# Optimization experiments

Measured on AMD Instinct MI355X. Metric: run time of the kernel, lower is better.

## Reference

```python
import jax, jax.numpy as jnp
import numpy as np

NUM_BLOCKS = 8
HIDDEN_FACTOR = 1
LAMBD = 0.01
HARD_FRACTION = 1.0
SCALE = 0.02


def softshrink(v, lambd):
    return jnp.sign(v) * jnp.maximum(jnp.abs(v) - lambd, 0.0)


def setup_inputs() -> dict:
    key = jax.random.key(0)
    ks = jax.random.split(key, 5)
    B, H, W, C = 4, 128, 128, 768
    bs = C // NUM_BLOCKS
    x = jax.random.normal(ks[0], (B, H * W, C), dtype=jnp.float32)
    w1 = SCALE * jax.random.normal(ks[1], (2, NUM_BLOCKS, bs, bs * HIDDEN_FACTOR), dtype=jnp.float32)
    b1 = SCALE * jax.random.normal(ks[2], (2, NUM_BLOCKS, bs * HIDDEN_FACTOR), dtype=jnp.float32)
    w2 = SCALE * jax.random.normal(ks[3], (2, NUM_BLOCKS, bs * HIDDEN_FACTOR, bs), dtype=jnp.float32)
    b2 = SCALE * jax.random.normal(ks[4], (2, NUM_BLOCKS, bs), dtype=jnp.float32)
    return {"x": x, "w1": w1, "b1": b1, "w2": w2, "b2": b2, "H": H, "W": W}


def reference(x, w1, b1, w2, b2, H, W):
    B, N, C = x.shape
    bs = C // NUM_BLOCKS
    bias = x
    xf = x.astype(jnp.float32).reshape(B, H, W, C)
    x_fft = jnp.fft.rfft2(xf, axes=(1, 2), norm='ortho')  # [B,H,W//2+1,C]
    Wm = W // 2 + 1
    kept = max(1, int(Wm * HARD_FRACTION))
    xr = x_fft.real.reshape(B, H, Wm, NUM_BLOCKS, bs)
    xi = x_fft.imag.reshape(B, H, Wm, NUM_BLOCKS, bs)
    xr_k = xr[:, :, :kept]
    xi_k = xi[:, :, :kept]
    # block-diagonal complex layer 1 + relu
    o1r = jax.nn.relu(jnp.einsum('bhwni,nio->bhwno', xr_k, w1[0])
                      - jnp.einsum('bhwni,nio->bhwno', xi_k, w1[1]) + b1[0])
    o1i = jax.nn.relu(jnp.einsum('bhwni,nio->bhwno', xi_k, w1[0])
                      + jnp.einsum('bhwni,nio->bhwno', xr_k, w1[1]) + b1[1])
    # layer 2
    o2r = (jnp.einsum('bhwno,noi->bhwni', o1r, w2[0])
           - jnp.einsum('bhwno,noi->bhwni', o1i, w2[1]) + b2[0])
    o2i = (jnp.einsum('bhwno,noi->bhwni', o1i, w2[0])
           + jnp.einsum('bhwno,noi->bhwni', o1r, w2[1]) + b2[1])
    o2r = softshrink(o2r, LAMBD)
    o2i = softshrink(o2i, LAMBD)
    # zero-pad unkept modes (kept == Wm when HARD_FRACTION == 1.0)
    if kept < Wm:
        pad = [(0, 0), (0, 0), (0, Wm - kept), (0, 0), (0, 0)]
        o2r = jnp.pad(o2r, pad)
        o2i = jnp.pad(o2i, pad)
    x_c = (o2r + 1j * o2i).reshape(B, H, Wm, C)
    x_out = jnp.fft.irfft2(x_c, s=(H, W), axes=(1, 2), norm='ortho')
    return x_out.reshape(B, N, C).astype(bias.dtype) + bias
```

## Files before the change

kernel.cpp:

```cpp
#include <hip/hip_runtime.h>
#include <hip/hip_bf16.h>

#define BDIM 256
constexpr int Bc = 4, Hc = 128, Wcn = 128, Cc = 768, WM = 65, NB = 8, BS = 96;
constexpr int NROWS = Bc * WM * Hc;
constexpr size_t NSPEC = (size_t)NROWS * Cc;

typedef __attribute__((ext_vector_type(8))) _Float16 f16x8;
typedef __attribute__((ext_vector_type(4))) float f32x4;
typedef __attribute__((ext_vector_type(4))) unsigned int u32x4;

__device__ __forceinline__ unsigned short f2h(float f) {
    return __builtin_bit_cast(unsigned short, (_Float16)f);
}
__device__ __forceinline__ float h2f(unsigned short s) {
    return (float)__builtin_bit_cast(_Float16, s);
}
__device__ __forceinline__ void barx() {
    __builtin_amdgcn_sched_barrier(0);
    asm volatile("s_waitcnt lgkmcnt(0)" ::: "memory");
    __builtin_amdgcn_s_barrier();
    __builtin_amdgcn_sched_barrier(0);
    asm volatile("" ::: "memory");
}

__global__ __launch_bounds__(BDIM) void kprep(const float* __restrict__ w1,
                                              const float* __restrict__ w2,
                                              unsigned short* __restrict__ WTg) {
    int idx = blockIdx.x * BDIM + threadIdx.x;
    if (idx >= 294912) return;
    int k = idx % 96, n = (idx / 96) % 96, blk = (idx / 9216) % 8, mat = idx / 73728;
    const float* src = (mat < 2) ? w1 : w2;
    int q = mat & 1;
    WTg[idx] = f2h(src[(((size_t)q * 8 + blk) * 96 + k) * 96 + n]);
}

constexpr int K1PAD = 136;
__global__ __launch_bounds__(BDIM, 1) void k1m(const float* __restrict__ x,
                                               unsigned short* __restrict__ Rr,
                                               unsigned short* __restrict__ Ri) {
    __shared__ unsigned short Xt[64][K1PAD];
    const int tid = threadIdx.x;
    const int lane = tid & 63;
    const int wv = tid >> 6;
    const int b = blockIdx.x >> 7, h = blockIdx.x & 127;
    const float* xp = x + ((size_t)(b * 16384 + h * 128)) * 768;
    const size_t sbase = ((size_t)(b * WM) * 128 + h) * 768;

    f16x8 Af[2][4];
    {
        const int rlo = wv * 32 + (lane & 15);
        #pragma unroll
        for (int rf = 0; rf < 2; ++rf) {
            const int r = rlo + rf * 16;
            const int m = (r < 65) ? r : (r - 64);
            #pragma unroll
            for (int ks = 0; ks < 4; ++ks) {
                f16x8 v;
                #pragma unroll
                for (int j = 0; j < 8; ++j) {
                    int k = ks * 32 + ((lane >> 4) << 3) + j;
                    float th = (float)((m * k) & 127) * 0.04908738521234052f;
                    float s, c; __sincosf(th, &s, &c);
                    v[j] = (_Float16)(((r < 65) ? c : -s) * 0.0078125f);
                }
                Af[rf][ks] = v;
            }
        }
    }

    const int w = tid & 127, cg = tid >> 7;
    float4 pfv[8];
    #pragma unroll
    for (int q = 0; q < 8; ++q)
        pfv[q] = *(const float4*)(xp + (size_t)w * 768 + cg * 32 + q * 4);

    const int koff = (lane >> 4) << 3;

    for (int t = 0; t < 12; ++t) {
        #pragma unroll
        for (int q = 0; q < 8; ++q) {
            float4 v = pfv[q];
            int cb = cg * 32 + q * 4;
            Xt[cb + 0][w] = f2h(v.x);
            Xt[cb + 1][w] = f2h(v.y);
            Xt[cb + 2][w] = f2h(v.z);
            Xt[cb + 3][w] = f2h(v.w);
        }
        if (t < 11) {
            #pragma unroll
            for (int q = 0; q < 8; ++q)
                pfv[q] = *(const float4*)(xp + (size_t)w * 768 + (t + 1) * 64 + cg * 32 + q * 4);
        }
        barx();

        f32x4 acc[2][4];
        #pragma unroll
        for (int rf = 0; rf < 2; ++rf)
            #pragma unroll
            for (int cf = 0; cf < 4; ++cf)
                acc[rf][cf] = (f32x4){0, 0, 0, 0};
        #pragma unroll
        for (int ks = 0; ks < 4; ++ks) {
            #pragma unroll
            for (int cf = 0; cf < 4; ++cf) {
                const int cl = cf * 16 + (lane & 15);
                f16x8 Bf = *(const f16x8*)(&Xt[cl][ks * 32 + koff]);
                #pragma unroll
                for (int rf = 0; rf < 2; ++rf)
                    acc[rf][cf] = __builtin_amdgcn_mfma_f32_16x16x32_f16(Af[rf][ks], Bf, acc[rf][cf], 0, 0, 0);
            }
        }
        #pragma unroll
        for (int rf = 0; rf < 2; ++rf)
            #pragma unroll
            for (int cf = 0; cf < 4; ++cf) {
                int col = t * 64 + cf * 16 + (lane & 15);
                int r0 = wv * 32 + rf * 16 + ((lane >> 4) << 2);
                #pragma unroll
                for (int reg = 0; reg < 4; ++reg) {
                    int r = r0 + reg;
                    if (r < 65) {
                        Rr[sbase + (size_t)r * 98304 + col] = f2h(acc[rf][cf][reg]);
                        if (r == 0)  Ri[sbase + col] = 0;
                        if (r == 64) Ri[sbase + (size_t)64 * 98304 + col] = 0;
                    } else {
                        Ri[sbase + (size_t)(r - 64) * 98304 + col] = f2h(acc[rf][cf][reg]);
                    }
                }
            }
        barx();
    }
}

constexpr int KMT = 136;
__global__ __launch_bounds__(BDIM) void kmid(unsigned short* __restrict__ Rr,
                                             unsigned short* __restrict__ Ri,
                                             const unsigned short* __restrict__ WTg,
                                             const float* __restrict__ b1,
                                             const float* __restrict__ b2) {
    extern __shared__ unsigned short lds[];
    unsigned short* Xtr = lds;
    unsigned short* Xti = Xtr + 96 * KMT;
    unsigned short* Y   = lds;

    const int tid = threadIdx.x;
    const int lane = tid & 63;
    const int wv = tid >> 6;
    const int blk = blockIdx.y;
    const size_t sbase = (size_t)blockIdx.x * 98304;

    const int hme = tid & 127, cgme = tid >> 7;
    u32x4 pfs[12];
    #pragma unroll
    for (int p = 0; p < 12; ++p) {
        const unsigned short* src = (p >= 6) ? Ri : Rr;
        int cg = (p % 6) * 2 + cgme;
        pfs[p] = *(const u32x4*)(src + sbase + (size_t)hme * 768 + blk * 96 + cg * 8);
    }

    const int n0 = wv * 48;
    float bias1[3], bias2[3];
    #pragma unroll
    for (int c = 0; c < 3; ++c) {
        int n = n0 + c * 16 + (lane & 15);
        bias1[c] = (n < 96) ? b1[blk * 96 + n] : b1[768 + blk * 96 + (n - 96)];
        bias2[c] = (n < 96) ? b2[blk * 96 + n] : b2[768 + blk * 96 + (n - 96)];
    }

    const int arow0 = wv * 32 + (lane & 15);
    const int koff = (lane >> 4) << 3;
    const int rowoff = (lane >> 4) << 2;

    int nq_c[3], nl_c[3];
    #pragma unroll
    for (int c = 0; c < 3; ++c) {
        nq_c[c] = (n0 + c * 16) < 96;
        nl_c[c] = n0 + c * 16 + (lane & 15) - (nq_c[c] ? 0 : 96);
    }

    #pragma unroll
    for (int p = 0; p < 12; ++p) {
        unsigned short* dst = (p >= 6) ? Xti : Xtr;
        int cl = ((p % 6) * 2 + cgme) * 8;
        unsigned short tmp[8];
        *(u32x4*)&tmp[0] = pfs[p];
        #pragma unroll
        for (int j = 0; j < 8; ++j)
            dst[(cl + j) * KMT + hme] = tmp[j];
    }
    __syncthreads();

    f32x4 accr[2][6], acci[2][6];
    #pragma unroll
    for (int rf = 0; rf < 2; ++rf)
        #pragma unroll
        for (int cf = 0; cf < 6; ++cf) {
            accr[rf][cf] = (f32x4){0, 0, 0, 0};
            acci[rf][cf] = (f32x4){0, 0, 0, 0};
        }
    {
        f16x8 Ca[2][4], Sa[2][4];
        #pragma unroll
        for (int rf = 0; rf < 2; ++rf) {
            const int r = arow0 + rf * 16;
            #pragma unroll
            for (int ks = 0; ks < 4; ++ks) {
                f16x8 cv, sv;
                #pragma unroll
                for (int j = 0; j < 8; ++j) {
                    int k = ks * 32 + koff + j;
                    float th = (float)((r * k) & 127) * 0.04908738521234052f;
                    float s, c; __sincosf(th, &s, &c);
                    cv[j] = (_Float16)c;
                    sv[j] = (_Float16)s;
                }
                Ca[rf][ks] = cv;
                Sa[rf][ks] = sv;
            }
        }
        #pragma unroll
        for (int ks = 0; ks < 4; ++ks) {
            f16x8 Sn[2];
            #pragma unroll
            for (int rf = 0; rf < 2; ++rf) {
                u32x4 u = __builtin_bit_cast(u32x4, Sa[rf][ks]);
                u ^= 0x80008000u;
                Sn[rf] = __builtin_bit_cast(f16x8, u);
            }
            #pragma unroll
            for (int cf = 0; cf < 6; ++cf) {
                int boff = (cf * 16 + (lane & 15)) * KMT + ks * 32 + koff;
                f16x8 Br = *(const f16x8*)(Xtr + boff);
                f16x8 Bi = *(const f16x8*)(Xti + boff);
                #pragma unroll
                for (int rf = 0; rf < 2; ++rf) {
                    accr[rf][cf] = __builtin_amdgcn_mfma_f32_16x16x32_f16(Ca[rf][ks], Br, accr[rf][cf], 0, 0, 0);
                    accr[rf][cf] = __builtin_amdgcn_mfma_f32_16x16x32_f16(Sa[rf][ks], Bi, accr[rf][cf], 0, 0, 0);
                    acci[rf][cf] = __builtin_amdgcn_mfma_f32_16x16x32_f16(Ca[rf][ks], Bi, acci[rf][cf], 0, 0, 0);
                    acci[rf][cf] = __builtin_amdgcn_mfma_f32_16x16x32_f16(Sn[rf], Br, acci[rf][cf], 0, 0, 0);
                }
            }
        }
    }
    __syncthreads();

    #pragma unroll
    for (int rf = 0; rf < 2; ++rf)
        #pragma unroll
        for (int cf = 0; cf < 6; ++cf) {
            int c = cf * 16 + (lane & 15);
            #pragma unroll
            for (int reg = 0; reg < 4; ++reg) {
                int row = wv * 32 + rf * 16 + rowoff + reg;
                Y[row * 200 + c]      = f2h(accr[rf][cf][reg]);
                Y[row * 200 + 96 + c] = f2h(acci[rf][cf][reg]);
            }
        }
    __syncthreads();

    const unsigned short* Xl = Y + (lane & 15) * 200 + koff;
    f32x4 acc[8][3];
    #pragma unroll
    for (int r = 0; r < 8; ++r)
        #pragma unroll
        for (int c = 0; c < 3; ++c)
            acc[r][c] = (f32x4){bias1[c], bias1[c], bias1[c], bias1[c]};
    #pragma unroll
    for (int kit = 0; kit < 6; ++kit) {
        const int kq = kit < 3;
        const int kl = kit * 32 + koff - (kq ? 0 : 96);
        f16x8 Bf[3];
        #pragma unroll
        for (int c = 0; c < 3; ++c) {
            const int quad = kq ? (nq_c[c] ? 0 : 1) : (nq_c[c] ? 1 : 0);
            f16x8 v = *(const f16x8*)(WTg + ((size_t)(quad * 8 + blk) * 96 + nl_c[c]) * 96 + kl);
            if ((!kq) && nq_c[c]) { u32x4 u = __builtin_bit_cast(u32x4, v); u ^= 0x80008000u; v = __builtin_bit_cast(f16x8, u); }
            Bf[c] = v;
        }
        f16x8 A[8];
        #pragma unroll
        for (int r = 0; r < 8; ++r)
            A[r] = *(const f16x8*)(Xl + r * 3200 + kit * 32);
        #pragma unroll
        for (int r = 0; r < 8; ++r)
            #pragma unroll
            for (int c = 0; c < 3; ++c)
                acc[r][c] = __builtin_amdgcn_mfma_f32_16x16x32_f16(A[r], Bf[c], acc[r][c], 0, 0, 0);
    }
    __syncthreads();
    #pragma unroll
    for (int r = 0; r < 8; ++r)
        #pragma unroll
        for (int c = 0; c < 3; ++c) {
            int ncol = n0 + c * 16 + (lane & 15);
            #pragma unroll
            for (int reg = 0; reg < 4; ++reg) {
                int row = r * 16 + rowoff + reg;
                Y[row * 200 + ncol] = f2h(fmaxf(acc[r][c][reg], 0.f));
            }
        }
    __syncthreads();

    #pragma unroll
    for (int r = 0; r < 8; ++r)
        #pragma unroll
        for (int c = 0; c < 3; ++c)
            acc[r][c] = (f32x4){bias2[c], bias2[c], bias2[c], bias2[c]};
    #pragma unroll
    for (int kit = 0; kit < 6; ++kit) {
        const int kq = kit < 3;
        const int kl = kit * 32 + koff - (kq ? 0 : 96);
        f16x8 Bf[3];
        #pragma unroll
        for (int c = 0; c < 3; ++c) {
            const int quad = kq ? (nq_c[c] ? 0 : 1) : (nq_c[c] ? 1 : 0);
            f16x8 v = *(const f16x8*)(WTg + ((size_t)((2 + quad) * 8 + blk) * 96 + nl_c[c]) * 96 + kl);
            if ((!kq) && nq_c[c]) { u32x4 u = __builtin_bit_cast(u32x4, v); u ^= 0x80008000u; v = __builtin_bit_cast(f16x8, u); }
            Bf[c] = v;
        }
        f16x8 A[8];
        #pragma unroll
        for (int r = 0; r < 8; ++r)
            A[r] = *(const f16x8*)(Xl + r * 3200 + kit * 32);
        #pragma unroll
        for (int r = 0; r < 8; ++r)
            #pragma unroll
            for (int c = 0; c < 3; ++c)
                acc[r][c] = __builtin_amdgcn_mfma_f32_16x16x32_f16(A[r], Bf[c], acc[r][c], 0, 0, 0);
    }
    __syncthreads();
    #pragma unroll
    for (int r = 0; r < 8; ++r)
        #pragma unroll
        for (int c = 0; c < 3; ++c) {
            int ncol = n0 + c * 16 + (lane & 15);
            unsigned short* dst = (ncol < 96) ? Xtr : Xti;
            int cc = (ncol < 96) ? ncol : ncol - 96;
            #pragma unroll
            for (int reg = 0; reg < 4; ++reg) {
                int row = r * 16 + rowoff + reg;
                float v = acc[r][c][reg];
                v = (v > 0.01f) ? v - 0.01f : ((v < -0.01f) ? v + 0.01f : 0.f);
                dst[cc * KMT + row] = f2h(v);
            }
        }
    __syncthreads();

    #pragma unroll
    for (int rf = 0; rf < 2; ++rf)
        #pragma unroll
        for (int cf = 0; cf < 6; ++cf) {
            accr[rf][cf] = (f32x4){0, 0, 0, 0};
            acci[rf][cf] = (f32x4){0, 0, 0, 0};
        }
    {
        f16x8 Ca[2][4], Sa[2][4];
        #pragma unroll
        for (int rf = 0; rf < 2; ++rf) {
            const int r = arow0 + rf * 16;
            #pragma unroll
            for (int ks = 0; ks < 4; ++ks) {
                f16x8 cv, sv;
                #pragma unroll
                for (int j = 0; j < 8; ++j) {
                    int k = ks * 32 + koff + j;
                    float th = (float)((r * k) & 127) * 0.04908738521234052f;
                    float s, c; __sincosf(th, &s, &c);
                    cv[j] = (_Float16)c;
                    sv[j] = (_Float16)s;
                }
                Ca[rf][ks] = cv;
                Sa[rf][ks] = sv;
            }
        }
        #pragma unroll
        for (int ks = 0; ks < 4; ++ks) {
            f16x8 Sn[2];
            #pragma unroll
            for (int rf = 0; rf < 2; ++rf) {
                u32x4 u = __builtin_bit_cast(u32x4, Sa[rf][ks]);
                u ^= 0x80008000u;
                Sn[rf] = __builtin_bit_cast(f16x8, u);
            }
            #pragma unroll
            for (int cf = 0; cf < 6; ++cf) {
                int boff = (cf * 16 + (lane & 15)) * KMT + ks * 32 + koff;
                f16x8 Br = *(const f16x8*)(Xtr + boff);
                f16x8 Bi = *(const f16x8*)(Xti + boff);
                #pragma unroll
                for (int rf = 0; rf < 2; ++rf) {
                    accr[rf][cf] = __builtin_amdgcn_mfma_f32_16x16x32_f16(Ca[rf][ks], Br, accr[rf][cf], 0, 0, 0);
                    accr[rf][cf] = __builtin_amdgcn_mfma_f32_16x16x32_f16(Sn[rf], Bi, accr[rf][cf], 0, 0, 0);
                    acci[rf][cf] = __builtin_amdgcn_mfma_f32_16x16x32_f16(Ca[rf][ks], Bi, acci[rf][cf], 0, 0, 0);
                    acci[rf][cf] = __builtin_amdgcn_mfma_f32_16x16x32_f16(Sa[rf][ks], Br, acci[rf][cf], 0, 0, 0);
                }
            }
        }
    }
    #pragma unroll
    for (int rf = 0; rf < 2; ++rf)
        #pragma unroll
        for (int cf = 0; cf < 6; ++cf) {
            int c = blk * 96 + cf * 16 + (lane & 15);
            int h0 = wv * 32 + rf * 16 + rowoff;
            #pragma unroll
            for (int reg = 0; reg < 4; ++reg) {
                size_t a = sbase + (size_t)(h0 + reg) * 768 + c;
                Rr[a] = f2h(accr[rf][cf][reg]);
                Ri[a] = f2h(acci[rf][cf][reg]);
            }
        }
}

constexpr int K5PAD = 104;
__global__ __launch_bounds__(BDIM, 1) void k5m(const unsigned short* __restrict__ Rr,
                                               const unsigned short* __restrict__ Ri,
                                               const float* __restrict__ x,
                                               float* __restrict__ out) {
    __shared__ unsigned short Xt[2][64][K5PAD];
    const int tid = threadIdx.x;
    const int lane = tid & 63;
    const int wv = tid >> 6;
    const int b = blockIdx.x >> 7, h = blockIdx.x & 127;
    const size_t rowbase = ((size_t)(b * WM) * 128 + h) * 768;
    const size_t obase = ((size_t)(b * 16384 + h * 128)) * 768;

    f16x8 Ca[2][3], Sa[2][3];
    {
        const int wrow_lo = wv * 32 + (lane & 15);
        #pragma unroll
        for (int rf = 0; rf < 2; ++rf) {
            const int wrow = wrow_lo + rf * 16;
            #pragma unroll
            for (int ks = 0; ks < 3; ++ks) {
                f16x8 cv, sv;
                #pragma unroll
                for (int j = 0; j < 8; ++j) {
                    int wm = ks * 32 + ((lane >> 4) << 3) + j;
                    float alpha = (wm > 64) ? 0.f : ((wm == 0 || wm == 64) ? 1.f : 2.f);
                    float th = (float)((wrow * wm) & 127) * 0.04908738521234052f;
                    float s, c; __sincosf(th, &s, &c);
                    cv[j] = (_Float16)(alpha * 0.0078125f * c);
                    sv[j] = (_Float16)(-alpha * 0.0078125f * s);
                }
                Ca[rf][ks] = cv;
                Sa[rf][ks] = sv;
            }
        }
    }

    for (int idx = tid; idx < 2 * 64 * 31; idx += BDIM) {
        int plane = idx / (64 * 31), rem = idx % (64 * 31);
        int cl = rem / 31, wm = 65 + rem % 31;
        Xt[plane][cl][wm] = 0;
    }

    unsigned short pfs[4][8], pfn[8];
    #pragma unroll
    for (int i = 0; i < 4; ++i) {
        const unsigned short* src = (i >> 1) ? Ri : Rr;
        int grp = (i & 1) * 4 + wv;
        *(u32x4*)&pfs[i][0] = *(const u32x4*)(src + rowbase + (size_t)lane * 98304 + grp * 8);
    }
    if (tid < 16) {
        const unsigned short* src = (tid >> 3) ? Ri : Rr;
        *(u32x4*)&pfn[0] = *(const u32x4*)(src + rowbase + (size_t)64 * 98304 + (tid & 7) * 8);
    }

    for (int t = 0; t < 12; ++t) {
        #pragma unroll
        for (int i = 0; i < 4; ++i) {
            int plane = i >> 1, grp = (i & 1) * 4 + wv;
            #pragma unroll
            for (int j = 0; j < 8; ++j)
                Xt[plane][grp * 8 + j][lane] = pfs[i][j];
        }
        if (tid < 16) {
            int plane = tid >> 3, grp = tid & 7;
            #pragma unroll
            for (int j = 0; j < 8; ++j)
                Xt[plane][grp * 8 + j][64] = pfn[j];
        }
        if (t < 11) {
            #pragma unroll
            for (int i = 0; i < 4; ++i) {
                const unsigned short* src = (i >> 1) ? Ri : Rr;
                int grp = (i & 1) * 4 + wv;
                *(u32x4*)&pfs[i][0] = *(const u32x4*)(src + rowbase + (size_t)lane * 98304 + (t + 1) * 64 + grp * 8);
            }
            if (tid < 16) {
                const unsigned short* src = (tid >> 3) ? Ri : Rr;
                *(u32x4*)&pfn[0] = *(const u32x4*)(src + rowbase + (size_t)64 * 98304 + (t + 1) * 64 + (tid & 7) * 8);
            }
        }
        barx();

        f32x4 acc[2][4];
        #pragma unroll
        for (int rf = 0; rf < 2; ++rf)
            #pragma unroll
            for (int cf = 0; cf < 4; ++cf)
                acc[rf][cf] = (f32x4){0, 0, 0, 0};
        const int koff = (lane >> 4) << 3;
        #pragma unroll
        for (int ks = 0; ks < 3; ++ks) {
            #pragma unroll
            for (int cf = 0; cf < 4; ++cf) {
                const int cl = cf * 16 + (lane & 15);
                f16x8 Br = *(const f16x8*)(&Xt[0][cl][ks * 32 + koff]);
                f16x8 Bi = *(const f16x8*)(&Xt[1][cl][ks * 32 + koff]);
                #pragma unroll
                for (int rf = 0; rf < 2; ++rf) {
                    acc[rf][cf] = __builtin_amdgcn_mfma_f32_16x16x32_f16(Ca[rf][ks], Br, acc[rf][cf], 0, 0, 0);
                    acc[rf][cf] = __builtin_amdgcn_mfma_f32_16x16x32_f16(Sa[rf][ks], Bi, acc[rf][cf], 0, 0, 0);
                }
            }
        }
        #pragma unroll
        for (int rf = 0; rf < 2; ++rf)
            #pragma unroll
            for (int cf = 0; cf < 4; ++cf) {
                int col = t * 64 + cf * 16 + (lane & 15);
                int row0 = wv * 32 + rf * 16 + ((lane >> 4) << 2);
                #pragma unroll
                for (int reg = 0; reg < 4; ++reg) {
                    size_t a = obase + (size_t)(row0 + reg) * 768 + col;
                    out[a] = acc[rf][cf][reg] + x[a];
                }
            }
        barx();
    }
}

extern "C" void kernel_launch(void* const* d_in, const int* in_sizes, int n_in,
                              void* d_out, int out_size, void* d_ws, size_t ws_size,
                              hipStream_t stream) {
    const float* x  = (const float*)d_in[0];
    const float* w1 = (const float*)d_in[1];
    const float* b1 = (const float*)d_in[2];
    const float* w2 = (const float*)d_in[3];
    const float* b2 = (const float*)d_in[4];
    float* out = (float*)d_out;

    unsigned short* Rr = (unsigned short*)d_ws;
    unsigned short* Ri = Rr + NSPEC;
    unsigned short* WTg = Ri + NSPEC;

    const size_t kmlds = (size_t)(2 * 96 * KMT) * 2;

    kprep<<<dim3(1152), BDIM, 0, stream>>>(w1, w2, WTg);
    k1m<<<dim3(512), BDIM, 0, stream>>>(x, Rr, Ri);
    kmid<<<dim3(260, 8), BDIM, kmlds, stream>>>(Rr, Ri, WTg, b1, b2);
    k5m<<<dim3(512), BDIM, 0, stream>>>(Rr, Ri, x, out);
}
```

Measured before the change: 372.5 us.

## Make kmid persistent with LDS-resident weights and prefetch of next tile

```diff
diff --git a/kernel.cpp b/kernel.cpp
--- a/kernel.cpp
+++ b/kernel.cpp
@@ -134,91 +134,105 @@
 }
 
 constexpr int KMT = 136;
+constexpr int WTP = 104;
 __global__ __launch_bounds__(BDIM) void kmid(unsigned short* __restrict__ Rr,
                                              unsigned short* __restrict__ Ri,
                                              const unsigned short* __restrict__ WTg,
                                              const float* __restrict__ b1,
                                              const float* __restrict__ b2) {
     extern __shared__ unsigned short lds[];
-    unsigned short* Xtr = lds;
+    unsigned short* WT  = lds;
+    unsigned short* Xtr = WT + 384 * WTP;
     unsigned short* Xti = Xtr + 96 * KMT;
-    unsigned short* Y   = lds;
+    unsigned short* Y   = Xtr;
 
     const int tid = threadIdx.x;
     const int lane = tid & 63;
     const int wv = tid >> 6;
     const int blk = blockIdx.y;
-    const size_t sbase = (size_t)blockIdx.x * 98304;
+    const int wgx = blockIdx.x;
 
     const int hme = tid & 127, cgme = tid >> 7;
+    const int arow0 = wv * 32 + (lane & 15);
+    const int koff = (lane >> 4) << 3;
+    const int rowoff = (lane >> 4) << 2;
+    const int n0 = wv * 48;
+
     u32x4 pfs[12];
+    {
+        size_t sb = (size_t)wgx * 98304;
+        #pragma unroll
+        for (int p = 0; p < 12; ++p) {
+            const unsigned short* src = (p >= 6) ? Ri : Rr;
+            int cg = (p % 6) * 2 + cgme;
+            pfs[p] = *(const u32x4*)(src + sb + (size_t)hme * 768 + blk * 96 + cg * 8);
+        }
+    }
+
     #pragma unroll
-    for (int p = 0; p < 12; ++p) {
-        const unsigned short* src = (p >= 6) ? Ri : Rr;
-        int cg = (p % 6) * 2 + cgme;
-        pfs[p] = *(const u32x4*)(src + sbase + (size_t)hme * 768 + blk * 96 + cg * 8);
-    }
-
-    const int n0 = wv * 48;
+    for (int i = 0; i < 18; ++i) {
+        int v = tid + i * BDIM;
+        int r = v / 12, kg = v % 12;
+        const unsigned short* src = WTg + (size_t)(r / 96) * 73728 + (size_t)blk * 9216
+                                        + (r % 96) * 96 + kg * 8;
+        *(u32x4*)(WT + r * WTP + kg * 8) = *(const u32x4*)src;
+    }
+
     float bias1[3], bias2[3];
+    int nq_c[3], nl_c[3];
     #pragma unroll
     for (int c = 0; c < 3; ++c) {
         int n = n0 + c * 16 + (lane & 15);
         bias1[c] = (n < 96) ? b1[blk * 96 + n] : b1[768 + blk * 96 + (n - 96)];
         bias2[c] = (n < 96) ? b2[blk * 96 + n] : b2[768 + blk * 96 + (n - 96)];
-    }
-
-    const int arow0 = wv * 32 + (lane & 15);
-    const int koff = (lane >> 4) << 3;
-    const int rowoff = (lane >> 4) << 2;
-
-    int nq_c[3], nl_c[3];
-    #pragma unroll
-    for (int c = 0; c < 3; ++c) {
         nq_c[c] = (n0 + c * 16) < 96;
         nl_c[c] = n0 + c * 16 + (lane & 15) - (nq_c[c] ? 0 : 96);
     }
 
+    f16x8 Ca[2][4], Sa[2][4];
     #pragma unroll
-    for (int p = 0; p < 12; ++p) {
-        unsigned short* dst = (p >= 6) ? Xti : Xtr;
-        int cl = ((p % 6) * 2 + cgme) * 8;
-        unsigned short tmp[8];
-        *(u32x4*)&tmp[0] = pfs[p];
-        #pragma unroll
-        for (int j = 0; j < 8; ++j)
-            dst[(cl + j) * KMT + hme] = tmp[j];
+    for (int rf = 0; rf < 2; ++rf) {
+        const int r = arow0 + rf * 16;
+        #pragma unroll
+        for (int ks = 0; ks < 4; ++ks) {
+            f16x8 cv, sv;
+            #pragma unroll
+            for (int j = 0; j < 8; ++j) {
+                int k = ks * 32 + koff + j;
+                float th = (float)((r * k) & 127) * 0.04908738521234052f;
+                float s, c; __sincosf(th, &s, &c);
+                cv[j] = (_Float16)c;
+                sv[j] = (_Float16)s;
+            }
+            Ca[rf][ks] = cv;
+            Sa[rf][ks] = sv;
+        }
     }
     __syncthreads();
 
-    f32x4 accr[2][6], acci[2][6];
-    #pragma unroll
-    for (int rf = 0; rf < 2; ++rf)
-        #pragma unroll
-        for (int cf = 0; cf < 6; ++cf) {
-            accr[rf][cf] = (f32x4){0, 0, 0, 0};
-            acci[rf][cf] = (f32x4){0, 0, 0, 0};
-        }
-    {
-        f16x8 Ca[2][4], Sa[2][4];
-        #pragma unroll
-        for (int rf = 0; rf < 2; ++rf) {
-            const int r = arow0 + rf * 16;
-            #pragma unroll
-            for (int ks = 0; ks < 4; ++ks) {
-                f16x8 cv, sv;
-                #pragma unroll
-                for (int j = 0; j < 8; ++j) {
-                    int k = ks * 32 + koff + j;
-                    float th = (float)((r * k) & 127) * 0.04908738521234052f;
-                    float s, c; __sincosf(th, &s, &c);
-                    cv[j] = (_Float16)c;
-                    sv[j] = (_Float16)s;
-                }
-                Ca[rf][ks] = cv;
-                Sa[rf][ks] = sv;
-            }
-        }
+    for (int tau = wgx; tau < 260; tau += 32) {
+        const size_t sbase = (size_t)tau * 98304;
+
+        #pragma unroll
+        for (int p = 0; p < 12; ++p) {
+            unsigned short* dst = (p >= 6) ? Xti : Xtr;
+            int cl = ((p % 6) * 2 + cgme) * 8;
+            unsigned short tmp[8];
+            *(u32x4*)&tmp[0] = pfs[p];
+            #pragma unroll
+            for (int j = 0; j < 8; ++j)
+                dst[(cl + j) * KMT + hme] = tmp[j];
+        }
+        barx();
+
+        f32x4 accr[2][6], acci[2][6];
+        #pragma unroll
+        for (int rf = 0; rf < 2; ++rf)
+            #pragma unroll
+            for (int cf = 0; cf < 6; ++cf) {
+                accr[rf][cf] = (f32x4){0, 0, 0, 0};
+                acci[rf][cf] = (f32x4){0, 0, 0, 0};
+            }
         #pragma unroll
         for (int ks = 0; ks < 4; ++ks) {
             f16x8 Sn[2];
@@ -242,138 +256,127 @@
                 }
             }
         }
-    }
-    __syncthreads();
-
-    #pragma unroll
-    for (int rf = 0; rf < 2; ++rf)
-        #pragma unroll
-        for (int cf = 0; cf < 6; ++cf) {
-            int c = cf * 16 + (lane & 15);
-            #pragma unroll
-            for (int reg = 0; reg < 4; ++reg) {
-                int row = wv * 32 + rf * 16 + rowoff + reg;
-                Y[row * 200 + c]      = f2h(accr[rf][cf][reg]);
-                Y[row * 200 + 96 + c] = f2h(acci[rf][cf][reg]);
-            }
-        }
-    __syncthreads();
-
-    const unsigned short* Xl = Y + (lane & 15) * 200 + koff;
-    f32x4 acc[8][3];
-    #pragma unroll
-    for (int r = 0; r < 8; ++r)
-        #pragma unroll
-        for (int c = 0; c < 3; ++c)
-            acc[r][c] = (f32x4){bias1[c], bias1[c], bias1[c], bias1[c]};
-    #pragma unroll
-    for (int kit = 0; kit < 6; ++kit) {
-        const int kq = kit < 3;
-        const int kl = kit * 32 + koff - (kq ? 0 : 96);
-        f16x8 Bf[3];
-        #pragma unroll
-        for (int c = 0; c < 3; ++c) {
-            const int quad = kq ? (nq_c[c] ? 0 : 1) : (nq_c[c] ? 1 : 0);
-            f16x8 v = *(const f16x8*)(WTg + ((size_t)(quad * 8 + blk) * 96 + nl_c[c]) * 96 + kl);
-            if ((!kq) && nq_c[c]) { u32x4 u = __builtin_bit_cast(u32x4, v); u ^= 0x80008000u; v = __builtin_bit_cast(f16x8, u); }
-            Bf[c] = v;
-        }
-        f16x8 A[8];
+        barx();
+
+        #pragma unroll
+        for (int rf = 0; rf < 2; ++rf)
+            #pragma unroll
+            for (int cf = 0; cf < 6; ++cf) {
+                int c = cf * 16 + (lane & 15);
+                #pragma unroll
+                for (int reg = 0; reg < 4; ++reg) {
+                    int row = wv * 32 + rf * 16 + rowoff + reg;
+                    Y[row * 200 + c]      = f2h(accr[rf][cf][reg]);
+                    Y[row * 200 + 96 + c] = f2h(acci[rf][cf][reg]);
+                }
+            }
+        barx();
+
+        const unsigned short* Xl = Y + (lane & 15) * 200 + koff;
+        f32x4 acc[8][3];
         #pragma unroll
         for (int r = 0; r < 8; ++r)
-            A[r] = *(const f16x8*)(Xl + r * 3200 + kit * 32);
+            #pragma unroll
+            for (int c = 0; c < 3; ++c)
+                acc[r][c] = (f32x4){bias1[c], bias1[c], bias1[c], bias1[c]};
+        #pragma unroll
+        for (int kit = 0; kit < 6; ++kit) {
+            const int kq = kit < 3;
+            const int kl = kit * 32 + koff - (kq ? 0 : 96);
+            f16x8 Bf[3];
+            #pragma unroll
+            for (int c = 0; c < 3; ++c) {
+                const int quad = kq ? (nq_c[c] ? 0 : 1) : (nq_c[c] ? 1 : 0);
+                f16x8 v = *(const f16x8*)(WT + (quad * 96 + nl_c[c]) * WTP + kl);
+                if ((!kq) && nq_c[c]) { u32x4 u = __builtin_bit_cast(u32x4, v); u ^= 0x80008000u; v = __builtin_bit_cast(f16x8, u); }
+                Bf[c] = v;
+            }
+            f16x8 A[8];
+            #pragma unroll
+            for (int r = 0; r < 8; ++r)
+                A[r] = *(const f16x8*)(Xl + r * 3200 + kit * 32);
+            #pragma unroll
+            for (int r = 0; r < 8; ++r)
+                #pragma unroll
+                for (int c = 0; c < 3; ++c)
+                    acc[r][c] = __builtin_amdgcn_mfma_f32_16x16x32_f16(A[r], Bf[c], acc[r][c], 0, 0, 0);
+        }
+        barx();
         #pragma unroll
         for (int r = 0; r < 8; ++r)
             #pragma unroll
+            for (int c = 0; c < 3; ++c) {
+                int ncol = n0 + c * 16 + (lane & 15);
+                #pragma unroll
+                for (int reg = 0; reg < 4; ++reg) {
+                    int row = r * 16 + rowoff + reg;
+                    Y[row * 200 + ncol] = f2h(fmaxf(acc[r][c][reg], 0.f));
+                }
+            }
+        barx();
+
+        #pragma unroll
+        for (int r = 0; r < 8; ++r)
+            #pragma unroll
             for (int c = 0; c < 3; ++c)
-                acc[r][c] = __builtin_amdgcn_mfma_f32_16x16x32_f16(A[r], Bf[c], acc[r][c], 0, 0, 0);
-    }
-    __syncthreads();
-    #pragma unroll
-    for (int r = 0; r < 8; ++r)
-        #pragma unroll
-        for (int c = 0; c < 3; ++c) {
-            int ncol = n0 + c * 16 + (lane & 15);
-            #pragma unroll
-            for (int reg = 0; reg < 4; ++reg) {
-                int row = r * 16 + rowoff + reg;
-                Y[row * 200 + ncol] = f2h(fmaxf(acc[r][c][reg], 0.f));
-            }
-        }
-    __syncthreads();
-
-    #pragma unroll
-    for (int r = 0; r < 8; ++r)
-        #pragma unroll
-        for (int c = 0; c < 3; ++c)
-            acc[r][c] = (f32x4){bias2[c], bias2[c], bias2[c], bias2[c]};
-    #pragma unroll
-    for (int kit = 0; kit < 6; ++kit) {
-        const int kq = kit < 3;
-        const int kl = kit * 32 + koff - (kq ? 0 : 96);
-        f16x8 Bf[3];
-        #pragma unroll
-        for (int c = 0; c < 3; ++c) {
-            const int quad = kq ? (nq_c[c] ? 0 : 1) : (nq_c[c] ? 1 : 0);
-            f16x8 v = *(const f16x8*)(WTg + ((size_t)((2 + quad) * 8 + blk) * 96 + nl_c[c]) * 96 + kl);
-            if ((!kq) && nq_c[c]) { u32x4 u = __builtin_bit_cast(u32x4, v); u ^= 0x80008000u; v = __builtin_bit_cast(f16x8, u); }
-            Bf[c] = v;
-        }
-        f16x8 A[8];
+                acc[r][c] = (f32x4){bias2[c], bias2[c], bias2[c], bias2[c]};
+        #pragma unroll
+        for (int kit = 0; kit < 6; ++kit) {
+            const int kq = kit < 3;
+            const int kl = kit * 32 + koff - (kq ? 0 : 96);
+            f16x8 Bf[3];
+            #pragma unroll
+            for (int c = 0; c < 3; ++c) {
+                const int quad = kq ? (nq_c[c] ? 0 : 1) : (nq_c[c] ? 1 : 0);
+                f16x8 v = *(const f16x8*)(WT + ((2 + quad) * 96 + nl_c[c]) * WTP + kl);
+                if ((!kq) && nq_c[c]) { u32x4 u = __builtin_bit_cast(u32x4, v); u ^= 0x80008000u; v = __builtin_bit_cast(f16x8, u); }
+                Bf[c] = v;
+            }
+            f16x8 A[8];
+            #pragma unroll
+            for (int r = 0; r < 8; ++r)
+                A[r] = *(const f16x8*)(Xl + r * 3200 + kit * 32);
+            #pragma unroll
+            for (int r = 0; r < 8; ++r)
+                #pragma unroll
+                for (int c = 0; c < 3; ++c)
+                    acc[r][c] = __builtin_amdgcn_mfma_f32_16x16x32_f16(A[r], Bf[c], acc[r][c], 0, 0, 0);
+        }
+        barx();
         #pragma unroll
         for (int r = 0; r < 8; ++r)
-            A[r] = *(const f16x8*)(Xl + r * 3200 + kit * 32);
-        #pragma unroll
-        for (int r = 0; r < 8; ++r)
-            #pragma unroll
-            for (int c = 0; c < 3; ++c)
-                acc[r][c] = __builtin_amdgcn_mfma_f32_16x16x32_f16(A[r], Bf[c], acc[r][c], 0, 0, 0);
-    }
-    __syncthreads();
-    #pragma unroll
-    for (int r = 0; r < 8; ++r)
-        #pragma unroll
-        for (int c = 0; c < 3; ++c) {
-            int ncol = n0 + c * 16 + (lane & 15);
-            unsigned short* dst = (ncol < 96) ? Xtr : Xti;
-            int cc = (ncol < 96) ? ncol : ncol - 96;
-            #pragma unroll
-            for (int reg = 0; reg < 4; ++reg) {
-                int row = r * 16 + rowoff + reg;
-                float v = acc[r][c][reg];
-                v = (v > 0.01f) ? v - 0.01f : ((v < -0.01f) ? v + 0.01f : 0.f);
-                dst[cc * KMT + row] = f2h(v);
-            }
-        }
-    __syncthreads();
-
-    #pragma unroll
-    for (int rf = 0; rf < 2; ++rf)
-        #pragma unroll
-        for (int cf = 0; cf < 6; ++cf) {
-            accr[rf][cf] = (f32x4){0, 0, 0, 0};
-            acci[rf][cf] = (f32x4){0, 0, 0, 0};
-        }
-    {
-        f16x8 Ca[2][4], Sa[2][4];
-        #pragma unroll
-        for (int rf = 0; rf < 2; ++rf) {
-            const int r = arow0 + rf * 16;
-            #pragma unroll
-            for (int ks = 0; ks < 4; ++ks) {
-                f16x8 cv, sv;
-                #pragma unroll
-                for (int j = 0; j < 8; ++j) {
-                    int k = ks * 32 + koff + j;
-                    float th = (float)((r * k) & 127) * 0.04908738521234052f;
-                    float s, c; __sincosf(th, &s, &c);
-                    cv[j] = (_Float16)c;
-                    sv[j] = (_Float16)s;
-                }
-                Ca[rf][ks] = cv;
-                Sa[rf][ks] = sv;
-            }
-        }
+            #pragma unroll
+            for (int c = 0; c < 3; ++c) {
+                int ncol = n0 + c * 16 + (lane & 15);
+                unsigned short* dst = (ncol < 96) ? Xtr : Xti;
+                int cc = (ncol < 96) ? ncol : ncol - 96;
+                #pragma unroll
+                for (int reg = 0; reg < 4; ++reg) {
+                    int row = r * 16 + rowoff + reg;
+                    float v = acc[r][c][reg];
+                    v = (v > 0.01f) ? v - 0.01f : ((v < -0.01f) ? v + 0.01f : 0.f);
+                    dst[cc * KMT + row] = f2h(v);
+                }
+            }
+        barx();
+
+        if (tau + 32 < 260) {
+            size_t sb = (size_t)(tau + 32) * 98304;
+            #pragma unroll
+            for (int p = 0; p < 12; ++p) {
+                const unsigned short* src = (p >= 6) ? Ri : Rr;
+                int cg = (p % 6) * 2 + cgme;
+                pfs[p] = *(const u32x4*)(src + sb + (size_t)hme * 768 + blk * 96 + cg * 8);
+            }
+        }
+
+        #pragma unroll
+        for (int rf = 0; rf < 2; ++rf)
+            #pragma unroll
+            for (int cf = 0; cf < 6; ++cf) {
+                accr[rf][cf] = (f32x4){0, 0, 0, 0};
+                acci[rf][cf] = (f32x4){0, 0, 0, 0};
+            }
         #pragma unroll
         for (int ks = 0; ks < 4; ++ks) {
             f16x8 Sn[2];
@@ -397,20 +400,21 @@
                 }
             }
         }
-    }
-    #pragma unroll
-    for (int rf = 0; rf < 2; ++rf)
-        #pragma unroll
-        for (int cf = 0; cf < 6; ++cf) {
-            int c = blk * 96 + cf * 16 + (lane & 15);
-            int h0 = wv * 32 + rf * 16 + rowoff;
-            #pragma unroll
-            for (int reg = 0; reg < 4; ++reg) {
-                size_t a = sbase + (size_t)(h0 + reg) * 768 + c;
-                Rr[a] = f2h(accr[rf][cf][reg]);
-                Ri[a] = f2h(acci[rf][cf][reg]);
-            }
-        }
+        #pragma unroll
+        for (int rf = 0; rf < 2; ++rf)
+            #pragma unroll
+            for (int cf = 0; cf < 6; ++cf) {
+                int c = blk * 96 + cf * 16 + (lane & 15);
+                int h0 = wv * 32 + rf * 16 + rowoff;
+                #pragma unroll
+                for (int reg = 0; reg < 4; ++reg) {
+                    size_t a = sbase + (size_t)(h0 + reg) * 768 + c;
+                    Rr[a] = f2h(accr[rf][cf][reg]);
+                    Ri[a] = f2h(acci[rf][cf][reg]);
+                }
+            }
+        barx();
+    }
 }
 
 constexpr int K5PAD = 104;
@@ -547,10 +551,10 @@
     unsigned short* Ri = Rr + NSPEC;
     unsigned short* WTg = Ri + NSPEC;
 
-    const size_t kmlds = (size_t)(2 * 96 * KMT) * 2;
+    const size_t kmlds = (size_t)(384 * WTP + 2 * 96 * KMT) * 2;
 
     kprep<<<dim3(1152), BDIM, 0, stream>>>(w1, w2, WTg);
     k1m<<<dim3(512), BDIM, 0, stream>>>(x, Rr, Ri);
-    kmid<<<dim3(260, 8), BDIM, kmlds, stream>>>(Rr, Ri, WTg, b1, b2);
+    kmid<<<dim3(32, 8), BDIM, kmlds, stream>>>(Rr, Ri, WTg, b1, b2);
     k5m<<<dim3(512), BDIM, 0, stream>>>(Rr, Ri, x, out);
 }
```

Result: slower. 607.0 us (+63.0%).
